# Performance work log

Hardware: AMD Instinct MI355X
Metric: run time of the kernel (lower is better)

## Reference

```python
import jax, jax.numpy as jnp
import numpy as np

KEEP_RATIO = 0.3
ALPHA, BETA, GAMMA, SMOOTH = 0.3, 0.7, 1.33, 1e-6
LOVASZ_W = 0.2


def _bce_with_logits(x, t):
    # stable binary_cross_entropy_with_logits, reduction='none'
    return jnp.maximum(x, 0.0) - x * t + jnp.log1p(jnp.exp(-jnp.abs(x)))


def _ohem_image(loss_i, tgt_i, tis_i, k_all):
    # loss_i/tgt_i/tis_i: [P] per-image flattened
    P = loss_i.shape[0]
    pos = tgt_i * tis_i                       # 1.0 where kept positive
    n_pos = jnp.sum(pos).astype(jnp.int32)
    neg_mask = (tgt_i == 0) & (tis_i == 1)
    n_remain = jnp.maximum(0, k_all - n_pos)
    # top-n_remain negative losses via full descending sort + rank mask
    neg_vals = jnp.where(neg_mask, loss_i, -jnp.inf)
    neg_sorted = -jnp.sort(-neg_vals)         # descending
    ranks = jnp.arange(P)
    valid = (ranks < n_remain) & jnp.isfinite(neg_sorted)
    neg_sum = jnp.sum(jnp.where(valid, neg_sorted, 0.0))
    n_neg_kept = jnp.sum(valid).astype(jnp.int32)
    pos_sum = jnp.sum(loss_i * pos)
    cnt = n_pos + n_neg_kept
    # fallback when nothing kept: hardest pixel inside tissue (or pixel 0)
    tis_vals = jnp.where(tis_i == 1, loss_i, -jnp.inf)
    has_tissue = jnp.any(tis_i == 1)
    fallback = jnp.where(has_tissue, jnp.max(tis_vals), loss_i[0])
    return jnp.where(cnt > 0, (pos_sum + neg_sum) / jnp.maximum(cnt, 1), fallback)


def _lovasz_image(log_flat, lab_flat):
    # binary Lovasz hinge, per image
    signs = 2.0 * lab_flat - 1.0
    errors = 1.0 - log_flat * signs
    order = jnp.argsort(-errors)              # descending by error
    errors_sorted = errors[order]
    gt_sorted = lab_flat[order]
    p = jnp.sum(gt_sorted)
    intersection = p - jnp.cumsum(gt_sorted)
    union = p + jnp.cumsum(1.0 - gt_sorted)
    jaccard = 1.0 - intersection / union
    n = gt_sorted.shape[0] - p
    grad = jnp.where(n > 0,
                     jnp.concatenate([jaccard[:1], jaccard[1:] - jaccard[:-1]]),
                     jaccard)
    return jnp.dot(jax.nn.relu(errors_sorted), grad)


def _forward(logits, targets, tissue_mask):
    t = targets.astype(jnp.float32)
    B = logits.shape[0]
    lf = logits.reshape(B, -1)                # [B, P]
    tf = t.reshape(B, -1)
    mf = tissue_mask.reshape(B, -1)
    P = lf.shape[1]
    k_all = max(1, int(P * KEEP_RATIO))       # static

    # --- OHEM BCE ---
    bce = _bce_with_logits(lf, tf) * mf
    ohem_i = jax.vmap(lambda l, tg, ms: _ohem_image(l, tg, ms, k_all))(bce, tf, mf)
    ohem_term = jnp.mean(ohem_i)

    # --- focal Tversky (per image) ---
    probs = jax.nn.sigmoid(lf)
    tp = jnp.sum(probs * tf, axis=1)
    fn = jnp.sum((1.0 - probs) * tf, axis=1)
    fp = jnp.sum(probs * (1.0 - tf), axis=1)
    tversky = (tp + SMOOTH) / (tp + ALPHA * fn + BETA * fp + SMOOTH)
    ft_i = (1.0 - tversky) ** GAMMA

    # --- Lovasz hinge (per image) ---
    lov_i = jax.vmap(_lovasz_image)(lf, tf)

    # masked mean over images that contain positives
    posb = jnp.sum(tf, axis=1) > 0
    npos = jnp.sum(posb)
    denom = jnp.maximum(npos, 1).astype(lf.dtype)
    ft_term = jnp.sum(jnp.where(posb, ft_i, 0.0)) / denom
    lov_term = jnp.sum(jnp.where(posb, lov_i, 0.0)) / denom
    return ohem_term + jnp.where(npos > 0, ft_term + LOVASZ_W * lov_term, 0.0)


def setup_inputs() -> dict:
    key = jax.random.key(0)
    k1, k2 = jax.random.split(key)
    B, H, W = 16, 768, 768
    logits = jax.random.normal(k1, (B, 1, H, W), dtype=jnp.float32)
    targets = jax.random.randint(k2, (B, 1, H, W), 0, 2, dtype=jnp.int32)
    tissue_mask = jnp.ones((B, 1, H, W), dtype=jnp.float32)
    return {"logits": logits, "targets": targets, "tissue_mask": tissue_mask}


def reference(logits, targets, tissue_mask):
    return _forward(logits, targets, tissue_mask)
```

## Files before the change

kernel.cpp:

```cpp
#include <hip/hip_runtime.h>
#include <math.h>

#define BB 16
#define PP (768*768)
#define NBINS 4096
#define CHUNKS 96
#define KALL 176947

#define LOV_LO (-17.0f)
#define LOV_RANGE 34.0f

typedef unsigned long long u64;

struct PAcc { float pos_sum, pos_w, tpx, sprx, mx, sum_t, n_tis, bce0; };
struct AccR { float lov_i, ft_i, ohem_i; unsigned posb; };

__device__ inline float wred_sum(float v) {
  #pragma unroll
  for (int o = 32; o > 0; o >>= 1) v += __shfl_down(v, o, 64);
  return v;
}
__device__ inline float wred_max(float v) {
  #pragma unroll
  for (int o = 32; o > 0; o >>= 1) v = fmaxf(v, __shfl_down(v, o, 64));
  return v;
}

__global__ __launch_bounds__(256) void k_main(const float* __restrict__ logits,
                                              const int* __restrict__ targets,
                                              const float* __restrict__ mask,
                                              PAcc* __restrict__ pacc,
                                              unsigned* __restrict__ partial1,
                                              unsigned* __restrict__ partial3)
{
  const int b = blockIdx.y;
  const int chunk = blockIdx.x;
  __shared__ unsigned hist1[NBINS];
  __shared__ unsigned hist3p[NBINS / 2];
  __shared__ float wsum[4][8];
  for (int i = threadIdx.x; i < NBINS; i += 256) hist1[i] = 0u;
  for (int i = threadIdx.x; i < NBINS / 2; i += 256) hist3p[i] = 0u;
  __syncthreads();

  const float4* l4 = (const float4*)(logits + (size_t)b * PP);
  const int4*   t4 = (const int4*)(targets + (size_t)b * PP);
  const float4* m4 = (const float4*)(mask + (size_t)b * PP);

  const float lov_scale = (float)NBINS / LOV_RANGE;

  float pos_sum = 0.f, pos_w = 0.f, tpa = 0.f, spra = 0.f, mx = 0.f;
  float sum_t = 0.f, n_tis = 0.f, bce0 = 0.f;

  if (chunk == 0 && threadIdx.x == 0) {
    float l = logits[(size_t)b * PP];
    float tf = (float)targets[(size_t)b * PP];
    float m = mask[(size_t)b * PP];
    float ex = __expf(-fabsf(l));
    bce0 = (fmaxf(l, 0.f) + __logf(1.f + ex) - l * tf) * m;
  }

  const int per_chunk4 = (PP / CHUNKS) / 4;
  const int base4 = chunk * per_chunk4;
  const int iters = per_chunk4 / 256;

  for (int it = 0; it < iters; ++it) {
    int i = base4 + it * 256 + threadIdx.x;
    float4 lv = l4[i]; int4 tv = t4[i]; float4 mv = m4[i];
    float ls[4] = {lv.x, lv.y, lv.z, lv.w};
    int   ts[4] = {tv.x, tv.y, tv.z, tv.w};
    float ms[4] = {mv.x, mv.y, mv.z, mv.w};
    #pragma unroll
    for (int c = 0; c < 4; ++c) {
      float l = ls[c]; int ti = ts[c]; float tf = (float)ti; float m = ms[c];
      float ex = __expf(-fabsf(l));
      float lg = __logf(1.f + ex);
      float loss = (fmaxf(l, 0.f) + lg - l * tf) * m;
      float posw = tf * m;
      pos_sum = fmaf(loss, posw, pos_sum);
      pos_w  += posw;
      float pr = ((l >= 0.f) ? 1.f : ex) * __builtin_amdgcn_rcpf(1.f + ex);
      spra += pr;
      tpa = fmaf(pr, tf, tpa);
      sum_t += tf;
      bool tis = (m == 1.0f);
      if (tis) { n_tis += 1.f; mx = fmaxf(mx, loss); }
      float s = fmaf(2.f, tf, -1.f);
      float e = fmaf(-l, s, 1.f);
      int bin = (int)((e - LOV_LO) * lov_scale);
      bin = bin < 0 ? 0 : (bin > NBINS - 1 ? NBINS - 1 : bin);
      atomicAdd(&hist1[bin], 1u | ((unsigned)ti << 16));
      if ((ti == 0) & !tis)
        atomicAdd(&hist3p[bin >> 1], 1u << ((bin & 1) << 4));
    }
  }

  {
    float v0 = wred_sum(pos_sum), v1 = wred_sum(pos_w), v2 = wred_sum(tpa);
    float v3 = wred_sum(spra), v4 = wred_max(mx), v5 = wred_sum(sum_t);
    float v6 = wred_sum(n_tis), v7 = wred_sum(bce0);
    int w = threadIdx.x >> 6, lane = threadIdx.x & 63;
    if (lane == 0) {
      wsum[w][0] = v0; wsum[w][1] = v1; wsum[w][2] = v2; wsum[w][3] = v3;
      wsum[w][4] = v4; wsum[w][5] = v5; wsum[w][6] = v6; wsum[w][7] = v7;
    }
  }
  __syncthreads();
  if (threadIdx.x == 0) {
    PAcc r;
    r.pos_sum = wsum[0][0] + wsum[1][0] + wsum[2][0] + wsum[3][0];
    r.pos_w   = wsum[0][1] + wsum[1][1] + wsum[2][1] + wsum[3][1];
    r.tpx     = wsum[0][2] + wsum[1][2] + wsum[2][2] + wsum[3][2];
    r.sprx    = wsum[0][3] + wsum[1][3] + wsum[2][3] + wsum[3][3];
    r.mx      = fmaxf(fmaxf(wsum[0][4], wsum[1][4]), fmaxf(wsum[2][4], wsum[3][4]));
    r.sum_t   = wsum[0][5] + wsum[1][5] + wsum[2][5] + wsum[3][5];
    r.n_tis   = wsum[0][6] + wsum[1][6] + wsum[2][6] + wsum[3][6];
    r.bce0    = wsum[0][7] + wsum[1][7] + wsum[2][7] + wsum[3][7];
    pacc[(size_t)b * CHUNKS + chunk] = r;
  }

  {
    unsigned* d1 = partial1 + ((size_t)b * CHUNKS + chunk) * NBINS;
    for (int i = threadIdx.x; i < NBINS; i += 256) d1[i] = hist1[i];
    unsigned* d3 = partial3 + ((size_t)b * CHUNKS + chunk) * (NBINS / 2);
    for (int i = threadIdx.x; i < NBINS / 2; i += 256) d3[i] = hist3p[i];
  }
}

__global__ __launch_bounds__(256) void k_reduce(const unsigned* __restrict__ partial1,
                                                const unsigned* __restrict__ partial3,
                                                u64* __restrict__ ghist,
                                                const PAcc* __restrict__ pacc,
                                                PAcc* __restrict__ accImg,
                                                unsigned* __restrict__ ticket)
{
  const int img = blockIdx.y;
  const int slice = blockIdx.x;
  const int bin = slice * 256 + threadIdx.x;
  const unsigned* s1 = partial1 + (size_t)img * CHUNKS * NBINS + bin;
  const unsigned* s3 = partial3 + (size_t)img * CHUNKS * (NBINS / 2) + (bin >> 1);
  const unsigned sh3 = (bin & 1) << 4;
  unsigned c = 0, q = 0, n0 = 0;
  #pragma unroll 4
  for (int p = 0; p < CHUNKS; ++p) {
    unsigned v = s1[(size_t)p * NBINS];
    c += v & 0xFFFFu; q += v >> 16;
    n0 += (s3[(size_t)p * (NBINS / 2)] >> sh3) & 0xFFFFu;
  }
  unsigned negtis = (c - q) - n0;
  ghist[(size_t)img * NBINS + bin] =
      (u64)c | ((u64)q << 20) | ((u64)negtis << 40);

  if (slice == 0 && threadIdx.x < 128) {
    int t = threadIdx.x;
    PAcc v;
    if (t < CHUNKS) v = pacc[(size_t)img * CHUNKS + t];
    else { v.pos_sum = v.pos_w = v.tpx = v.sprx = v.mx = v.sum_t = v.n_tis = v.bce0 = 0.f; }
    v.pos_sum = wred_sum(v.pos_sum); v.pos_w = wred_sum(v.pos_w);
    v.tpx = wred_sum(v.tpx); v.sprx = wred_sum(v.sprx);
    v.mx = wred_max(v.mx); v.sum_t = wred_sum(v.sum_t);
    v.n_tis = wred_sum(v.n_tis); v.bce0 = wred_sum(v.bce0);
    __shared__ PAcc half[2];
    if ((t & 63) == 0) half[t >> 6] = v;
    __syncthreads();
    if (t == 0) {
      PAcc r = half[0], h = half[1];
      r.pos_sum += h.pos_sum; r.pos_w += h.pos_w; r.tpx += h.tpx; r.sprx += h.sprx;
      r.mx = fmaxf(r.mx, h.mx); r.sum_t += h.sum_t; r.n_tis += h.n_tis; r.bce0 += h.bce0;
      accImg[img] = r;
    }
  }
  if (slice == 0 && img == 0 && threadIdx.x == 0) *ticket = 0u;
}

__global__ __launch_bounds__(256) void k_scan(const PAcc* __restrict__ accImg,
                                              const u64* __restrict__ ghist,
                                              AccR* __restrict__ acc,
                                              unsigned* __restrict__ ticket,
                                              float* __restrict__ out)
{
  const int b = blockIdx.x;
  const int t = threadIdx.x;
  __shared__ unsigned sA[256], sB[256], sC[256];
  __shared__ float sf[256], sg[256];
  __shared__ unsigned ng_total_sh;

  const u64* gh = ghist + (size_t)b * NBINS;
  const PAcc a = accImg[b];

  const unsigned sum_t = (unsigned)a.sum_t;
  const float p = (float)sum_t;
  const bool has_pos = sum_t > 0;
  const unsigned n_neg_total = (unsigned)PP - sum_t;
  const int CH = NBINS / 256;
  const float lov_d = LOV_RANGE / (float)NBINS;

  int n_pos = (int)a.pos_w;
  int n_remain = KALL - n_pos; if (n_remain < 0) n_remain = 0;

  u64 loc[16];
  unsigned tc = 0, tq = 0, tn = 0;
  #pragma unroll
  for (int k = 0; k < 16; ++k) {
    u64 v = gh[NBINS - 1 - (t * CH + k)];
    loc[k] = v;
    tc += (unsigned)(v & 0xFFFFFu);
    tq += (unsigned)((v >> 20) & 0xFFFFFu);
    tn += (unsigned)((v >> 40) & 0xFFFFFu);
  }
  sA[t] = tc; sB[t] = tq; sC[t] = tn;
  __syncthreads();
  if (t == 0) {
    unsigned aI = 0, aC = 0, aN = 0;
    for (int i = 0; i < 256; i++) {
      unsigned ci = sA[i], qi = sB[i], ni = sC[i];
      sA[i] = aI; sB[i] = aC; sC[i] = aN;
      aI += ci; aC += qi; aN += ni;
    }
    ng_total_sh = aN;
  }
  __syncthreads();

  float lov_local = 0.f, ns_local = 0.f;
  {
    unsigned I = sA[t], C = sB[t], NG = sC[t];
    float Jprev = has_pos ? (1.f - (p - (float)C) / (p + (float)I - (float)C)) : 0.f;
    #pragma unroll 4
    for (int k = 0; k < 16; ++k) {
      int j = NBINS - 1 - (t * CH + k);
      u64 v = loc[k];
      unsigned c = (unsigned)(v & 0xFFFFFu);
      if (c) {
        unsigned q = (unsigned)((v >> 20) & 0xFFFFFu);
        unsigned ng = (unsigned)((v >> 40) & 0xFFFFFu);
        float e = LOV_LO + ((float)j + 0.5f) * lov_d;
        if (has_pos) {
          float re = fmaxf(e, 0.f);
          if (n_neg_total > 0) {
            I += c; C += q;
            float Jb = 1.f - (p - (float)C) / (p + (float)I - (float)C);
            lov_local += re * (Jb - Jprev);
            Jprev = Jb;
          } else {
            double hi = (double)I + (double)c;
            double s = (hi * (hi + 1.0) - (double)I * ((double)I + 1.0)) * 0.5 / (double)p;
            lov_local += re * (float)s;
            I += c;
          }
        }
        if (n_remain > 0 && ng) {
          long long rem = (long long)n_remain - (long long)NG;
          unsigned take = rem <= 0 ? 0u : (rem >= (long long)ng ? ng : (unsigned)rem);
          if (take) {
            float l = e - 1.f;
            float nloss = fmaxf(l, 0.f) + __logf(1.f + __expf(-fabsf(l)));
            ns_local += (float)take * nloss;
          }
          NG += ng;
        }
      }
    }
  }
  sf[t] = lov_local; sg[t] = ns_local; __syncthreads();
  for (int off = 128; off > 0; off >>= 1) {
    if (t < off) { sf[t] += sf[t + off]; sg[t] += sg[t + off]; }
    __syncthreads();
  }

  if (t == 0) {
    float lov = sf[0];
    float neg_sum = sg[0];
    unsigned kept = (n_remain > 0)
        ? ((unsigned)n_remain < ng_total_sh ? (unsigned)n_remain : ng_total_sh) : 0u;
    float cnt = (float)n_pos + (float)kept;
    float ohem;
    if (cnt > 0.f) ohem = (a.pos_sum + neg_sum) / cnt;
    else ohem = (a.n_tis > 0.f) ? a.mx : a.bce0;
    float tp = a.tpx;
    float fn = p - tp;
    float fp = a.sprx - tp;
    float tv = (tp + 1e-6f) / (tp + 0.3f * fn + 0.7f * fp + 1e-6f);
    float ft = powf(fmaxf(1.f - tv, 0.f), 1.33f);
    acc[b].lov_i = lov; acc[b].ft_i = ft; acc[b].ohem_i = ohem;
    acc[b].posb = has_pos ? 1u : 0u;

    __threadfence();
    unsigned ret = atomicAdd(ticket, 1u);
    if (ret == BB - 1) {
      __threadfence();
      volatile AccR* va = acc;
      float os = 0.f, fts = 0.f, lvs = 0.f; int np = 0;
      for (int i = 0; i < BB; i++) {
        os += va[i].ohem_i;
        if (va[i].posb) { np++; fts += va[i].ft_i; lvs += va[i].lov_i; }
      }
      float denom = (np > 0) ? (float)np : 1.f;
      float r = os / (float)BB;
      if (np > 0) r += fts / denom + 0.2f * (lvs / denom);
      out[0] = r;
    }
  }
}

extern "C" void kernel_launch(void* const* d_in, const int* in_sizes, int n_in,
                              void* d_out, int out_size, void* d_ws, size_t ws_size,
                              hipStream_t stream) {
  const float* logits  = (const float*)d_in[0];
  const int*   targets = (const int*)d_in[1];
  const float* mask    = (const float*)d_in[2];
  float* out = (float*)d_out;

  char* ws = (char*)d_ws;
  AccR*     acc      = (AccR*)ws;
  unsigned* ticket   = (unsigned*)(ws + 256);
  PAcc*     accImg   = (PAcc*)(ws + 512);
  PAcc*     pacc     = (PAcc*)(ws + 1024);
  u64*      ghist    = (u64*)(ws + (64 << 10));
  unsigned* partial1 = (unsigned*)(ws + (1 << 20));
  unsigned* partial3 = (unsigned*)(ws + (1 << 20) + (size_t)BB * CHUNKS * NBINS * 4);
  (void)in_sizes; (void)n_in; (void)out_size; (void)ws_size;


  dim3 g1(CHUNKS, BB, 1);
  k_main<<<g1, 256, 0, stream>>>(logits, targets, mask, pacc, partial1, partial3);
  dim3 g2(NBINS / 256, BB, 1);
  k_reduce<<<g2, 256, 0, stream>>>(partial1, partial3, ghist, pacc, accImg, ticket);
  k_scan<<<BB, 256, 0, stream>>>(accImg, ghist, acc, ticket, out);
}
```

Baseline: 170.9 us.

## Halve histogram bins, skip empty negtis partials, split reduce across chunk groups

Halves the histogram resolution and raises the number of chunks per image. A per-chunk flag lets the main kernel skip writing, and the reduce skip reading, the non-tissue negative partial histogram when every pixel in the chunk is tissue. The reduce kernel now splits the chunk sum across four wave groups for more parallelism, and the per-image scalar reduction moves into the scan kernel. Coarser bins may reduce the accuracy of the Lovasz and OHEM approximations.

```diff
diff --git a/kernel.cpp b/kernel.cpp
--- a/kernel.cpp
+++ b/kernel.cpp
@@ -3,8 +3,10 @@
 
 #define BB 16
 #define PP (768*768)
-#define NBINS 4096
-#define CHUNKS 96
+#define NBINS 2048
+#define CHUNKS 128
+#define PIXB (PP / CHUNKS)
+#define PC4  (PIXB / 4)
 #define KALL 176947
 
 #define LOV_LO (-17.0f)
@@ -31,13 +33,15 @@
                                               const float* __restrict__ mask,
                                               PAcc* __restrict__ pacc,
                                               unsigned* __restrict__ partial1,
-                                              unsigned* __restrict__ partial3)
+                                              unsigned* __restrict__ partial3,
+                                              unsigned* __restrict__ flags)
 {
   const int b = blockIdx.y;
   const int chunk = blockIdx.x;
   __shared__ unsigned hist1[NBINS];
   __shared__ unsigned hist3p[NBINS / 2];
   __shared__ float wsum[4][8];
+  __shared__ unsigned s_any3;
   for (int i = threadIdx.x; i < NBINS; i += 256) hist1[i] = 0u;
   for (int i = threadIdx.x; i < NBINS / 2; i += 256) hist3p[i] = 0u;
   __syncthreads();
@@ -59,38 +63,39 @@
     bce0 = (fmaxf(l, 0.f) + __logf(1.f + ex) - l * tf) * m;
   }
 
-  const int per_chunk4 = (PP / CHUNKS) / 4;
-  const int base4 = chunk * per_chunk4;
-  const int iters = per_chunk4 / 256;
-
-  for (int it = 0; it < iters; ++it) {
-    int i = base4 + it * 256 + threadIdx.x;
-    float4 lv = l4[i]; int4 tv = t4[i]; float4 mv = m4[i];
-    float ls[4] = {lv.x, lv.y, lv.z, lv.w};
-    int   ts[4] = {tv.x, tv.y, tv.z, tv.w};
-    float ms[4] = {mv.x, mv.y, mv.z, mv.w};
-    #pragma unroll
-    for (int c = 0; c < 4; ++c) {
-      float l = ls[c]; int ti = ts[c]; float tf = (float)ti; float m = ms[c];
-      float ex = __expf(-fabsf(l));
-      float lg = __logf(1.f + ex);
-      float loss = (fmaxf(l, 0.f) + lg - l * tf) * m;
-      float posw = tf * m;
-      pos_sum = fmaf(loss, posw, pos_sum);
-      pos_w  += posw;
-      float pr = ((l >= 0.f) ? 1.f : ex) * __builtin_amdgcn_rcpf(1.f + ex);
-      spra += pr;
-      tpa = fmaf(pr, tf, tpa);
-      sum_t += tf;
-      bool tis = (m == 1.0f);
-      if (tis) { n_tis += 1.f; mx = fmaxf(mx, loss); }
-      float s = fmaf(2.f, tf, -1.f);
-      float e = fmaf(-l, s, 1.f);
-      int bin = (int)((e - LOV_LO) * lov_scale);
-      bin = bin < 0 ? 0 : (bin > NBINS - 1 ? NBINS - 1 : bin);
-      atomicAdd(&hist1[bin], 1u | ((unsigned)ti << 16));
-      if ((ti == 0) & !tis)
-        atomicAdd(&hist3p[bin >> 1], 1u << ((bin & 1) << 4));
+  const int base4 = chunk * PC4;
+
+  for (int it = 0; it < 5; ++it) {
+    int idx = it * 256 + threadIdx.x;
+    if (idx < PC4) {
+      int i = base4 + idx;
+      float4 lv = l4[i]; int4 tv = t4[i]; float4 mv = m4[i];
+      float ls[4] = {lv.x, lv.y, lv.z, lv.w};
+      int   ts[4] = {tv.x, tv.y, tv.z, tv.w};
+      float ms[4] = {mv.x, mv.y, mv.z, mv.w};
+      #pragma unroll
+      for (int c = 0; c < 4; ++c) {
+        float l = ls[c]; int ti = ts[c]; float tf = (float)ti; float m = ms[c];
+        float ex = __expf(-fabsf(l));
+        float lg = __logf(1.f + ex);
+        float loss = (fmaxf(l, 0.f) + lg - l * tf) * m;
+        float posw = tf * m;
+        pos_sum = fmaf(loss, posw, pos_sum);
+        pos_w  += posw;
+        float pr = ((l >= 0.f) ? 1.f : ex) * __builtin_amdgcn_rcpf(1.f + ex);
+        spra += pr;
+        tpa = fmaf(pr, tf, tpa);
+        sum_t += tf;
+        bool tis = (m == 1.0f);
+        if (tis) { n_tis += 1.f; mx = fmaxf(mx, loss); }
+        float s = fmaf(2.f, tf, -1.f);
+        float e = fmaf(-l, s, 1.f);
+        int bin = (int)((e - LOV_LO) * lov_scale);
+        bin = bin < 0 ? 0 : (bin > NBINS - 1 ? NBINS - 1 : bin);
+        atomicAdd(&hist1[bin], 1u | ((unsigned)ti << 16));
+        if ((ti == 0) & !tis)
+          atomicAdd(&hist3p[bin >> 1], 1u << ((bin & 1) << 4));
+      }
     }
   }
 
@@ -116,76 +121,105 @@
     r.n_tis   = wsum[0][6] + wsum[1][6] + wsum[2][6] + wsum[3][6];
     r.bce0    = wsum[0][7] + wsum[1][7] + wsum[2][7] + wsum[3][7];
     pacc[(size_t)b * CHUNKS + chunk] = r;
-  }
+    unsigned any3 = (r.n_tis != (float)PIXB) ? 1u : 0u;
+    s_any3 = any3;
+    flags[(size_t)b * CHUNKS + chunk] = any3;
+  }
+  __syncthreads();
 
   {
     unsigned* d1 = partial1 + ((size_t)b * CHUNKS + chunk) * NBINS;
     for (int i = threadIdx.x; i < NBINS; i += 256) d1[i] = hist1[i];
-    unsigned* d3 = partial3 + ((size_t)b * CHUNKS + chunk) * (NBINS / 2);
-    for (int i = threadIdx.x; i < NBINS / 2; i += 256) d3[i] = hist3p[i];
+    if (s_any3) {
+      unsigned* d3 = partial3 + ((size_t)b * CHUNKS + chunk) * (NBINS / 2);
+      for (int i = threadIdx.x; i < NBINS / 2; i += 256) d3[i] = hist3p[i];
+    }
   }
 }
 
 __global__ __launch_bounds__(256) void k_reduce(const unsigned* __restrict__ partial1,
                                                 const unsigned* __restrict__ partial3,
+                                                const unsigned* __restrict__ flags,
                                                 u64* __restrict__ ghist,
-                                                const PAcc* __restrict__ pacc,
-                                                PAcc* __restrict__ accImg,
-                                                unsigned* __restrict__ ticket)
+                                                unsigned* __restrict__ tickets)
 {
   const int img = blockIdx.y;
   const int slice = blockIdx.x;
-  const int bin = slice * 256 + threadIdx.x;
-  const unsigned* s1 = partial1 + (size_t)img * CHUNKS * NBINS + bin;
-  const unsigned* s3 = partial3 + (size_t)img * CHUNKS * (NBINS / 2) + (bin >> 1);
-  const unsigned sh3 = (bin & 1) << 4;
-  unsigned c = 0, q = 0, n0 = 0;
-  #pragma unroll 4
-  for (int p = 0; p < CHUNKS; ++p) {
+  const int t = threadIdx.x;
+  const int lane = t & 63, g = t >> 6;
+  const int bin = slice * 64 + lane;
+  __shared__ unsigned sC[256], sQ[256];
+  __shared__ unsigned short s_list[CHUNKS];
+  __shared__ int s_n;
+
+  const unsigned* s1 = partial1 + ((size_t)img * CHUNKS + (size_t)g * 32) * NBINS + bin;
+  unsigned c = 0, q = 0;
+  #pragma unroll 8
+  for (int p = 0; p < 32; ++p) {
     unsigned v = s1[(size_t)p * NBINS];
     c += v & 0xFFFFu; q += v >> 16;
-    n0 += (s3[(size_t)p * (NBINS / 2)] >> sh3) & 0xFFFFu;
-  }
-  unsigned negtis = (c - q) - n0;
-  ghist[(size_t)img * NBINS + bin] =
-      (u64)c | ((u64)q << 20) | ((u64)negtis << 40);
-
-  if (slice == 0 && threadIdx.x < 128) {
-    int t = threadIdx.x;
-    PAcc v;
-    if (t < CHUNKS) v = pacc[(size_t)img * CHUNKS + t];
-    else { v.pos_sum = v.pos_w = v.tpx = v.sprx = v.mx = v.sum_t = v.n_tis = v.bce0 = 0.f; }
-    v.pos_sum = wred_sum(v.pos_sum); v.pos_w = wred_sum(v.pos_w);
-    v.tpx = wred_sum(v.tpx); v.sprx = wred_sum(v.sprx);
-    v.mx = wred_max(v.mx); v.sum_t = wred_sum(v.sum_t);
-    v.n_tis = wred_sum(v.n_tis); v.bce0 = wred_sum(v.bce0);
-    __shared__ PAcc half[2];
-    if ((t & 63) == 0) half[t >> 6] = v;
-    __syncthreads();
-    if (t == 0) {
-      PAcc r = half[0], h = half[1];
-      r.pos_sum += h.pos_sum; r.pos_w += h.pos_w; r.tpx += h.tpx; r.sprx += h.sprx;
-      r.mx = fmaxf(r.mx, h.mx); r.sum_t += h.sum_t; r.n_tis += h.n_tis; r.bce0 += h.bce0;
-      accImg[img] = r;
-    }
-  }
-  if (slice == 0 && img == 0 && threadIdx.x == 0) *ticket = 0u;
-}
-
-__global__ __launch_bounds__(256) void k_scan(const PAcc* __restrict__ accImg,
+  }
+  sC[t] = c; sQ[t] = q;
+
+  if (t == 0) {
+    int n = 0;
+    for (int p = 0; p < CHUNKS; ++p) if (flags[(size_t)img * CHUNKS + p]) s_list[n++] = (unsigned short)p;
+    s_n = n;
+  }
+  __syncthreads();
+
+  if (t < 64) {
+    unsigned ct = sC[t] + sC[64 + t] + sC[128 + t] + sC[192 + t];
+    unsigned qt = sQ[t] + sQ[64 + t] + sQ[128 + t] + sQ[192 + t];
+    const int bn = slice * 64 + t;
+    unsigned n0 = 0;
+    const unsigned sh = (bn & 1) << 4;
+    for (int k = 0; k < s_n; ++k) {
+      int p = s_list[k];
+      n0 += (partial3[((size_t)img * CHUNKS + p) * (NBINS / 2) + (bn >> 1)] >> sh) & 0xFFFFu;
+    }
+    unsigned negtis = (ct - qt) - n0;
+    ghist[(size_t)img * NBINS + bn] = (u64)ct | ((u64)qt << 20) | ((u64)negtis << 40);
+  }
+  if (slice == 0 && img == 0 && t == 0) tickets[0] = 0u;
+}
+
+__global__ __launch_bounds__(256) void k_scan(const PAcc* __restrict__ pacc,
                                               const u64* __restrict__ ghist,
                                               AccR* __restrict__ acc,
-                                              unsigned* __restrict__ ticket,
+                                              unsigned* __restrict__ tickets,
                                               float* __restrict__ out)
 {
   const int b = blockIdx.x;
   const int t = threadIdx.x;
   __shared__ unsigned sA[256], sB[256], sC[256];
   __shared__ float sf[256], sg[256];
+  __shared__ PAcc halfw[4];
+  __shared__ PAcc aS;
   __shared__ unsigned ng_total_sh;
 
-  const u64* gh = ghist + (size_t)b * NBINS;
-  const PAcc a = accImg[b];
+  {
+    PAcc v;
+    v.pos_sum = v.pos_w = v.tpx = v.sprx = v.mx = v.sum_t = v.n_tis = v.bce0 = 0.f;
+    if (t < CHUNKS) v = pacc[(size_t)b * CHUNKS + t];
+    v.pos_sum = wred_sum(v.pos_sum); v.pos_w = wred_sum(v.pos_w);
+    v.tpx = wred_sum(v.tpx); v.sprx = wred_sum(v.sprx);
+    v.mx = wred_max(v.mx); v.sum_t = wred_sum(v.sum_t);
+    v.n_tis = wred_sum(v.n_tis); v.bce0 = wred_sum(v.bce0);
+    if ((t & 63) == 0) halfw[t >> 6] = v;
+    __syncthreads();
+    if (t == 0) {
+      PAcc r = halfw[0];
+      for (int w = 1; w < 4; ++w) {
+        PAcc h = halfw[w];
+        r.pos_sum += h.pos_sum; r.pos_w += h.pos_w; r.tpx += h.tpx; r.sprx += h.sprx;
+        r.mx = fmaxf(r.mx, h.mx); r.sum_t += h.sum_t; r.n_tis += h.n_tis; r.bce0 += h.bce0;
+      }
+      aS = r;
+    }
+    __syncthreads();
+  }
+  const PAcc a = aS;
 
   const unsigned sum_t = (unsigned)a.sum_t;
   const float p = (float)sum_t;
@@ -197,10 +231,11 @@
   int n_pos = (int)a.pos_w;
   int n_remain = KALL - n_pos; if (n_remain < 0) n_remain = 0;
 
-  u64 loc[16];
+  const u64* gh = ghist + (size_t)b * NBINS;
+  u64 loc[8];
   unsigned tc = 0, tq = 0, tn = 0;
   #pragma unroll
-  for (int k = 0; k < 16; ++k) {
+  for (int k = 0; k < 8; ++k) {
     u64 v = gh[NBINS - 1 - (t * CH + k)];
     loc[k] = v;
     tc += (unsigned)(v & 0xFFFFFu);
@@ -225,7 +260,7 @@
     unsigned I = sA[t], C = sB[t], NG = sC[t];
     float Jprev = has_pos ? (1.f - (p - (float)C) / (p + (float)I - (float)C)) : 0.f;
     #pragma unroll 4
-    for (int k = 0; k < 16; ++k) {
+    for (int k = 0; k < 8; ++k) {
       int j = NBINS - 1 - (t * CH + k);
       u64 v = loc[k];
       unsigned c = (unsigned)(v & 0xFFFFFu);
@@ -284,7 +319,7 @@
     acc[b].posb = has_pos ? 1u : 0u;
 
     __threadfence();
-    unsigned ret = atomicAdd(ticket, 1u);
+    unsigned ret = atomicAdd(&tickets[0], 1u);
     if (ret == BB - 1) {
       __threadfence();
       volatile AccR* va = acc;
@@ -311,18 +346,17 @@
 
   char* ws = (char*)d_ws;
   AccR*     acc      = (AccR*)ws;
-  unsigned* ticket   = (unsigned*)(ws + 256);
-  PAcc*     accImg   = (PAcc*)(ws + 512);
+  unsigned* tickets  = (unsigned*)(ws + 256);
   PAcc*     pacc     = (PAcc*)(ws + 1024);
-  u64*      ghist    = (u64*)(ws + (64 << 10));
-  unsigned* partial1 = (unsigned*)(ws + (1 << 20));
-  unsigned* partial3 = (unsigned*)(ws + (1 << 20) + (size_t)BB * CHUNKS * NBINS * 4);
+  unsigned* flags    = (unsigned*)(ws + (80 << 10));
+  u64*      ghist    = (u64*)(ws + (96 << 10));
+  unsigned* partial1 = (unsigned*)(ws + (512 << 10));
+  unsigned* partial3 = (unsigned*)(ws + (512 << 10) + (size_t)BB * CHUNKS * NBINS * 4);
   (void)in_sizes; (void)n_in; (void)out_size; (void)ws_size;
 
-
   dim3 g1(CHUNKS, BB, 1);
-  k_main<<<g1, 256, 0, stream>>>(logits, targets, mask, pacc, partial1, partial3);
-  dim3 g2(NBINS / 256, BB, 1);
-  k_reduce<<<g2, 256, 0, stream>>>(partial1, partial3, ghist, pacc, accImg, ticket);
-  k_scan<<<BB, 256, 0, stream>>>(accImg, ghist, acc, ticket, out);
-}
+  k_main<<<g1, 256, 0, stream>>>(logits, targets, mask, pacc, partial1, partial3, flags);
+  dim3 g2(NBINS / 64, BB, 1);
+  k_reduce<<<g2, 256, 0, stream>>>(partial1, partial3, flags, ghist, tickets);
+  k_scan<<<BB, 256, 0, stream>>>(pacc, ghist, acc, tickets, out);
+}
```

After: 163.0 us. -4.6%, faster.
